# Kernel tuning notes

Hardware: AMD Instinct MI355X
Metric: run time of the kernel (lower is better)

Reference implementation:

```python
import jax, jax.numpy as jnp
import numpy as np

DIM = 128
KERNEL = 7
NUM_HEADS = 4
HEAD_DIM = DIM // NUM_HEADS
SCALE = HEAD_DIM ** (-0.5)


def _nbhd_indices(size, k):
    # NATTEN edge-clamped neighborhood: start index so the k-window stays in bounds
    pos = jnp.arange(size)
    start = jnp.clip(pos - k // 2, 0, size - k)          # (size,)
    idx = start[:, None] + jnp.arange(k)[None, :]        # (size, k) absolute key index
    bias = idx - pos[:, None] + (k - 1)                  # (size, k) rpb index in [0, 2k-2]
    return idx, bias


def setup_inputs() -> dict:
    key = jax.random.key(0)
    ks = jax.random.split(key, 6)
    B, H, W = 4, 64, 64
    x = jax.random.normal(ks[0], (B, H, W, DIM), dtype=jnp.float32)
    w_qkv = jax.random.normal(ks[1], (DIM, 3 * DIM), dtype=jnp.float32) * (DIM ** -0.5)
    b_qkv = jax.random.normal(ks[2], (3 * DIM,), dtype=jnp.float32) * 0.02
    rpb = jax.random.normal(ks[3], (NUM_HEADS, 2 * KERNEL - 1, 2 * KERNEL - 1), dtype=jnp.float32) * 0.02
    w_proj = jax.random.normal(ks[4], (DIM, DIM), dtype=jnp.float32) * (DIM ** -0.5)
    b_proj = jax.random.normal(ks[5], (DIM,), dtype=jnp.float32) * 0.02
    return {"x": x, "w_qkv": w_qkv, "b_qkv": b_qkv, "rpb": rpb,
            "w_proj": w_proj, "b_proj": b_proj}


def reference(x, w_qkv, b_qkv, rpb, w_proj, b_proj):
    B, H, W, C = x.shape
    k = KERNEL
    # qkv projection; split order (3, heads, head_dim) matches torch reshape
    qkv = (x @ w_qkv + b_qkv).reshape(B, H, W, 3, NUM_HEADS, HEAD_DIM)
    q = jnp.transpose(qkv[..., 0, :, :], (0, 3, 1, 2, 4)) * SCALE  # (B,nh,H,W,hd)
    kk = jnp.transpose(qkv[..., 1, :, :], (0, 3, 1, 2, 4))
    v = jnp.transpose(qkv[..., 2, :, :], (0, 3, 1, 2, 4))

    idx_i, bias_i = _nbhd_indices(H, k)  # (H,k)
    idx_j, bias_j = _nbhd_indices(W, k)  # (W,k)

    # gather local k x k neighborhoods of keys/values: (B,nh,H,W,k,k,hd)
    II = idx_i[:, None, :, None]
    JJ = idx_j[None, :, None, :]
    k_nb = kk[:, :, II, JJ, :]
    v_nb = v[:, :, II, JJ, :]

    # QK + relative position bias gathered per offset
    attn = jnp.einsum('bnhwd,bnhwpqd->bnhwpq', q, k_nb)
    attn = attn + rpb[:, bias_i[:, None, :, None], bias_j[None, :, None, :]][None]

    # softmax over the k*k neighborhood
    attn = jax.nn.softmax(attn.reshape(B, NUM_HEADS, H, W, k * k), axis=-1)
    attn = attn.reshape(B, NUM_HEADS, H, W, k, k)

    out = jnp.einsum('bnhwpq,bnhwpqd->bnhwd', attn, v_nb)
    out = jnp.transpose(out, (0, 2, 3, 1, 4)).reshape(B, H, W, C)
    return out @ w_proj + b_proj
```

## Files before the change

### kernel.cpp

```cpp
#include <hip/hip_runtime.h>
#include <hip/hip_bf16.h>

typedef float f4 __attribute__((ext_vector_type(4)));
typedef float f32x4 __attribute__((ext_vector_type(4)));
typedef unsigned short u16x8 __attribute__((ext_vector_type(8)));
typedef short short8 __attribute__((ext_vector_type(8)));

#define QSCALE 0.17677669529663689f

__device__ inline float b2f(unsigned short u){
  union{unsigned int i; float f;} z; z.i = ((unsigned int)u)<<16; return z.f;
}
__device__ inline unsigned short f2b(float f){
  union{float f; unsigned int i;} z; z.f=f;
  unsigned int i = z.i;
  return (unsigned short)((i + 0x7FFFu + ((i>>16)&1u)) >> 16);
}

__global__ __launch_bounds__(256) void k_prep(const float* __restrict__ wq,
    const float* __restrict__ wp, unsigned short* __restrict__ wT,
    unsigned short* __restrict__ wpT)
{
  __shared__ float T[32][129];
  const int b = blockIdx.x, t = threadIdx.x;
  const float* src; unsigned short* dst; int N, n0;
  if (b < 12){ src = wq; dst = wT;  N = 384; n0 = b*32; }
  else       { src = wp; dst = wpT; N = 128; n0 = (b-12)*32; }
  for (int i = t; i < 4096; i += 256){
    int k = i >> 5, c = i & 31;
    T[c][k] = src[k*N + n0 + c];
  }
  __syncthreads();
  const int n = t >> 3, k0 = (t & 7) << 4;
#pragma unroll
  for (int e = 0; e < 2; ++e){
    u16x8 o;
#pragma unroll
    for (int j = 0; j < 8; ++j) o[j] = f2b(T[n][k0 + e*8 + j]);
    *(u16x8*)&dst[(n0+n)*128 + k0 + e*8] = o;
  }
}

__global__ __launch_bounds__(256) void k_qkv_mfma(const float* __restrict__ x,
    const unsigned short* __restrict__ wT, const float* __restrict__ bias,
    unsigned short* __restrict__ qo, unsigned short* __restrict__ ko,
    unsigned short* __restrict__ vo)
{
  __shared__ short lds[64*128 + 128*128];
  short* As = lds;
  short* Bs = lds + 64*128;
  const int t = threadIdx.x;
  const int m0 = blockIdx.x * 64;
  const int ny = blockIdx.y;
  const int n0 = ny * 128;

  for (int c = t; c < 1024; c += 256){
    int row = c >> 4, k0 = (c & 15) << 3;
    const float* p = &x[(m0+row)*128 + k0];
    f4 lo = *(const f4*)p, hi = *(const f4*)(p+4);
    u16x8 v;
    v[0]=f2b(lo[0]); v[1]=f2b(lo[1]); v[2]=f2b(lo[2]); v[3]=f2b(lo[3]);
    v[4]=f2b(hi[0]); v[5]=f2b(hi[1]); v[6]=f2b(hi[2]); v[7]=f2b(hi[3]);
    int byte = (row<<8) + (k0<<1);
    *(u16x8*)((char*)As + (byte ^ ((row&7)<<4))) = v;
  }
  for (int c = t; c < 2048; c += 256){
    int n = c >> 4, k0 = (c & 15) << 3;
    u16x8 v = *(const u16x8*)&wT[(n0+n)*128 + k0];
    int byte = (n<<8) + (k0<<1);
    *(u16x8*)((char*)Bs + (byte ^ ((n&7)<<4))) = v;
  }
  __syncthreads();

  const int w = t >> 6, l = t & 63;
  const int wm = (w >> 1) * 32, wn = (w & 1) * 64;
  const int lr = l & 15, lk = (l >> 4) << 3;
  f32x4 acc[2][4] = {};
#pragma unroll
  for (int k0 = 0; k0 < 128; k0 += 32){
    const int koff = k0 + lk;
    short8 a[2], bf[4];
#pragma unroll
    for (int fm = 0; fm < 2; ++fm){
      int row = wm + fm*16 + lr;
      int byte = (row<<8) + (koff<<1);
      a[fm] = *(short8*)((char*)As + (byte ^ ((row&7)<<4)));
    }
#pragma unroll
    for (int fn = 0; fn < 4; ++fn){
      int rn = wn + fn*16 + lr;
      int byte = (rn<<8) + (koff<<1);
      bf[fn] = *(short8*)((char*)Bs + (byte ^ ((rn&7)<<4)));
    }
#pragma unroll
    for (int fm = 0; fm < 2; ++fm)
#pragma unroll
      for (int fn = 0; fn < 4; ++fn)
        acc[fm][fn] = __builtin_amdgcn_mfma_f32_16x16x32_bf16(a[fm], bf[fn], acc[fm][fn], 0, 0, 0);
  }
  __syncthreads();

  unsigned short* C = (unsigned short*)lds;
  const float scale = (ny == 0) ? QSCALE : 1.0f;
#pragma unroll
  for (int fm = 0; fm < 2; ++fm)
#pragma unroll
    for (int fn = 0; fn < 4; ++fn){
      int col = wn + fn*16 + lr;
      float bv = bias[n0 + col];
#pragma unroll
      for (int r = 0; r < 4; ++r){
        int row = wm + fm*16 + ((l>>4)<<2) + r;
        C[row*136 + col] = f2b((acc[fm][fn][r] + bv) * scale);
      }
    }
  __syncthreads();
  unsigned short* dst = ny==0 ? qo : (ny==1 ? ko : vo);
  for (int c = t; c < 1024; c += 256){
    int row = c >> 4, k0 = (c & 15) << 3;
    *(u16x8*)&dst[(m0+row)*128 + k0] = *(u16x8*)&C[row*136 + k0];
  }
}

__global__ __launch_bounds__(256) void k_attn(
    const unsigned short* __restrict__ qg,
    const unsigned short* __restrict__ kg,
    const unsigned short* __restrict__ vg,
    const float* __restrict__ rpb,
    unsigned short* __restrict__ ao)
{
  __shared__ unsigned short ks[196*136];
  __shared__ unsigned short vs[196*136];
  __shared__ float rs[676];
  const int t = threadIdx.x;
  const int b = blockIdx.z;
  const int th0 = blockIdx.y * 8, tw0 = blockIdx.x * 8;
  const int bi0 = min(max(th0-3,0),50);
  const int bj0 = min(max(tw0-3,0),50);
  for (int c = t; c < 3136; c += 256){
    int tok = c >> 4, part = c & 15;
    int trow = tok/14;
    int gi = bi0 + trow;
    int gj = bj0 + (tok - trow*14);
    int go = ((b*64+gi)*64+gj)*128 + part*8;
    int lo = tok*136 + part*8;
    *(u16x8*)&ks[lo] = *(const u16x8*)&kg[go];
    *(u16x8*)&vs[lo] = *(const u16x8*)&vg[go];
  }
  for (int c = t; c < 676; c += 256) rs[c] = rpb[c];
  __syncthreads();

  const int lt = t >> 2, h = t & 3;
  const int ti = th0 + (lt >> 3), tj = tw0 + (lt & 7);
  const int si = min(max(ti-3,0),57), sj = min(max(tj-3,0),57);
  const int li = si - bi0, lj = sj - bj0;
  const int ri = si - ti + 6, rj = sj - tj + 6;

  float q[32];
  {
    int qb = ((b*64+ti)*64+tj)*128 + h*32;
#pragma unroll
    for (int j=0;j<4;++j){
      u16x8 u = *(const u16x8*)&qg[qb + j*8];
#pragma unroll
      for (int e=0;e<8;++e) q[j*8+e] = b2f(u[e]);
    }
  }
  float m = -1e30f, l = 0.f, o[32];
#pragma unroll
  for (int d=0; d<32; ++d) o[d] = 0.f;

  for (int pi=0; pi<7; ++pi){
    const int rowoff = (li+pi)*14;
    const float* rrow = &rs[h*169 + (ri+pi)*13 + rj];
    for (int pj=0; pj<7; ++pj){
      int lo = (rowoff + lj + pj)*136 + h*32;
      float s = rrow[pj];
#pragma unroll
      for (int j=0;j<4;++j){
        u16x8 kk = *(const u16x8*)&ks[lo + j*8];
#pragma unroll
        for (int e=0;e<8;++e) s += q[j*8+e]*b2f(kk[e]);
      }
      float mn = fmaxf(m, s);
      float sc = __expf(m - mn);
      float e  = __expf(s - mn);
      l = l*sc + e;
#pragma unroll
      for (int j=0;j<4;++j){
        u16x8 vv = *(const u16x8*)&vs[lo + j*8];
#pragma unroll
        for (int e2=0;e2<8;++e2){
          int d = j*8+e2;
          o[d] = o[d]*sc + e*b2f(vv[e2]);
        }
      }
      m = mn;
    }
  }
  float inv = 1.f / l;
  int ob = ((b*64+ti)*64+tj)*128 + h*32;
#pragma unroll
  for (int j=0;j<16;++j){
    *(unsigned int*)&ao[ob + 2*j] =
      (unsigned int)f2b(o[2*j]*inv) | ((unsigned int)f2b(o[2*j+1]*inv)<<16);
  }
}

__global__ __launch_bounds__(256) void k_proj_mfma(
    const unsigned short* __restrict__ a,
    const unsigned short* __restrict__ wpT, const float* __restrict__ bias,
    float* __restrict__ out)
{
  __shared__ short lds[64*128 + 128*128];
  short* As = lds;
  short* Bs = lds + 64*128;
  const int t = threadIdx.x;
  const int m0 = blockIdx.x * 64;

  for (int c = t; c < 1024; c += 256){
    int row = c >> 4, k0 = (c & 15) << 3;
    u16x8 v = *(const u16x8*)&a[(m0+row)*128 + k0];
    int byte = (row<<8) + (k0<<1);
    *(u16x8*)((char*)As + (byte ^ ((row&7)<<4))) = v;
  }
  for (int c = t; c < 2048; c += 256){
    int n = c >> 4, k0 = (c & 15) << 3;
    u16x8 v = *(const u16x8*)&wpT[n*128 + k0];
    int byte = (n<<8) + (k0<<1);
    *(u16x8*)((char*)Bs + (byte ^ ((n&7)<<4))) = v;
  }
  __syncthreads();

  const int w = t >> 6, l = t & 63;
  const int wm = (w >> 1) * 32, wn = (w & 1) * 64;
  const int lr = l & 15, lk = (l >> 4) << 3;
  f32x4 acc[2][4] = {};
#pragma unroll
  for (int k0 = 0; k0 < 128; k0 += 32){
    const int koff = k0 + lk;
    short8 afr[2], bf[4];
#pragma unroll
    for (int fm = 0; fm < 2; ++fm){
      int row = wm + fm*16 + lr;
      int byte = (row<<8) + (koff<<1);
      afr[fm] = *(short8*)((char*)As + (byte ^ ((row&7)<<4)));
    }
#pragma unroll
    for (int fn = 0; fn < 4; ++fn){
      int rn = wn + fn*16 + lr;
      int byte = (rn<<8) + (koff<<1);
      bf[fn] = *(short8*)((char*)Bs + (byte ^ ((rn&7)<<4)));
    }
#pragma unroll
    for (int fm = 0; fm < 2; ++fm)
#pragma unroll
      for (int fn = 0; fn < 4; ++fn)
        acc[fm][fn] = __builtin_amdgcn_mfma_f32_16x16x32_bf16(afr[fm], bf[fn], acc[fm][fn], 0, 0, 0);
  }
  __syncthreads();

  float* C = (float*)lds;
#pragma unroll
  for (int fm = 0; fm < 2; ++fm)
#pragma unroll
    for (int fn = 0; fn < 4; ++fn){
      int col = wn + fn*16 + lr;
      float bv = bias[col];
#pragma unroll
      for (int r = 0; r < 4; ++r){
        int row = wm + fm*16 + ((l>>4)<<2) + r;
        C[row*132 + col] = acc[fm][fn][r] + bv;
      }
    }
  __syncthreads();
  for (int c = t; c < 2048; c += 256){
    int row = c >> 5, k0 = (c & 31) << 2;
    *(f4*)&out[(m0+row)*128 + k0] = *(const f4*)&C[row*132 + k0];
  }
}

extern "C" void kernel_launch(void* const* d_in, const int* in_sizes, int n_in,
                              void* d_out, int out_size, void* d_ws, size_t ws_size,
                              hipStream_t stream) {
  const float* x      = (const float*)d_in[0];
  const float* w_qkv  = (const float*)d_in[1];
  const float* b_qkv  = (const float*)d_in[2];
  const float* rpb    = (const float*)d_in[3];
  const float* w_proj = (const float*)d_in[4];
  const float* b_proj = (const float*)d_in[5];
  float* out = (float*)d_out;

  unsigned short* qo  = (unsigned short*)d_ws;
  unsigned short* ko  = qo + 16384*128;
  unsigned short* vo  = ko + 16384*128;
  unsigned short* ao  = vo + 16384*128;
  unsigned short* wT  = ao + 16384*128;
  unsigned short* wpT = wT + 384*128;

  k_prep<<<16, 256, 0, stream>>>(w_qkv, w_proj, wT, wpT);
  k_qkv_mfma<<<dim3(256, 3), 256, 0, stream>>>(x, wT, b_qkv, qo, ko, vo);
  k_attn<<<dim3(8, 8, 4), 256, 0, stream>>>(qo, ko, vo, rpb, ao);
  k_proj_mfma<<<256, 256, 0, stream>>>(ao, wpT, b_proj, out);
}
```

Before: 53.16 us.

## Split attention blocks per head with head-major QKV layout and neighbor-parallel softmax

QKV outputs are written in head-major layout, so each attention block handles a single head and loads only that head's 14x14 K/V tile into a smaller LDS buffer. The grid grows from 256 to 1024 blocks, and each token's 49 neighbors are split across 4 lanes. Each lane computes a two-pass softmax (max first, then exp-sum) instead of an online rescale, and the partial results are reduced with shuffles. This raises occupancy and parallelism and removes the serial per-neighbor rescaling, at the cost of more shuffle traffic and redundant K/V halo loads across the per-head blocks.

```diff
diff --git a/kernel.cpp b/kernel.cpp
--- a/kernel.cpp
+++ b/kernel.cpp
@@ -118,7 +118,8 @@
   unsigned short* dst = ny==0 ? qo : (ny==1 ? ko : vo);
   for (int c = t; c < 1024; c += 256){
     int row = c >> 4, k0 = (c & 15) << 3;
-    *(u16x8*)&dst[(m0+row)*128 + k0] = *(u16x8*)&C[row*136 + k0];
+    int head = k0 >> 5, d0 = k0 & 31;
+    *(u16x8*)&dst[(head*16384 + m0 + row)*32 + d0] = *(u16x8*)&C[row*136 + k0];
   }
 }
 
@@ -129,28 +130,29 @@
     const float* __restrict__ rpb,
     unsigned short* __restrict__ ao)
 {
-  __shared__ unsigned short ks[196*136];
-  __shared__ unsigned short vs[196*136];
-  __shared__ float rs[676];
+  __shared__ unsigned short ks[196*40];
+  __shared__ unsigned short vs[196*40];
+  __shared__ float rs[169];
   const int t = threadIdx.x;
-  const int b = blockIdx.z;
+  const int b = blockIdx.z >> 2, h = blockIdx.z & 3;
   const int th0 = blockIdx.y * 8, tw0 = blockIdx.x * 8;
   const int bi0 = min(max(th0-3,0),50);
   const int bj0 = min(max(tw0-3,0),50);
-  for (int c = t; c < 3136; c += 256){
-    int tok = c >> 4, part = c & 15;
-    int trow = tok/14;
-    int gi = bi0 + trow;
-    int gj = bj0 + (tok - trow*14);
-    int go = ((b*64+gi)*64+gj)*128 + part*8;
-    int lo = tok*136 + part*8;
-    *(u16x8*)&ks[lo] = *(const u16x8*)&kg[go];
-    *(u16x8*)&vs[lo] = *(const u16x8*)&vg[go];
-  }
-  for (int c = t; c < 676; c += 256) rs[c] = rpb[c];
-  __syncthreads();
-
-  const int lt = t >> 2, h = t & 3;
+  const unsigned short* kb = kg + (h*16384 + b*4096)*32;
+  const unsigned short* vb = vg + (h*16384 + b*4096)*32;
+
+  for (int c = t; c < 784; c += 256){
+    int tok = c >> 2, ch = c & 3;
+    int trow = tok/14, tcol = tok - trow*14;
+    int g = ((bi0+trow)*64 + (bj0+tcol))*32 + ch*8;
+    int lo = tok*40 + ch*8;
+    *(u16x8*)&ks[lo] = *(const u16x8*)&kb[g];
+    *(u16x8*)&vs[lo] = *(const u16x8*)&vb[g];
+  }
+  for (int c = t; c < 169; c += 256) rs[c] = rpb[h*169 + c];
+  __syncthreads();
+
+  const int lt = t >> 2, p = t & 3;
   const int ti = th0 + (lt >> 3), tj = tw0 + (lt & 7);
   const int si = min(max(ti-3,0),57), sj = min(max(tj-3,0),57);
   const int li = si - bi0, lj = sj - bj0;
@@ -158,7 +160,7 @@
 
   float q[32];
   {
-    int qb = ((b*64+ti)*64+tj)*128 + h*32;
+    int qb = (h*16384 + b*4096 + ti*64 + tj)*32;
 #pragma unroll
     for (int j=0;j<4;++j){
       u16x8 u = *(const u16x8*)&qg[qb + j*8];
@@ -166,45 +168,58 @@
       for (int e=0;e<8;++e) q[j*8+e] = b2f(u[e]);
     }
   }
-  float m = -1e30f, l = 0.f, o[32];
+
+  float s[13]; int toks[13];
+  float mx = -1e30f;
+#pragma unroll
+  for (int it = 0; it < 13; ++it){
+    int n = p + (it << 2);
+    bool ok = (n < 49);
+    int nn = ok ? n : 48;
+    int pi = nn / 7, pj = nn - pi*7;
+    int tok = (li+pi)*14 + (lj+pj);
+    toks[it] = tok;
+    float acc = rs[(ri+pi)*13 + (rj+pj)];
+#pragma unroll
+    for (int j=0;j<4;++j){
+      u16x8 kk = *(const u16x8*)&ks[tok*40 + j*8];
+#pragma unroll
+      for (int e=0;e<8;++e) acc += q[j*8+e]*b2f(kk[e]);
+    }
+    s[it] = ok ? acc : -1e30f;
+    mx = fmaxf(mx, s[it]);
+  }
+  mx = fmaxf(mx, __shfl_xor(mx, 1));
+  mx = fmaxf(mx, __shfl_xor(mx, 2));
+
+  float l = 0.f, o[32];
 #pragma unroll
   for (int d=0; d<32; ++d) o[d] = 0.f;
-
-  for (int pi=0; pi<7; ++pi){
-    const int rowoff = (li+pi)*14;
-    const float* rrow = &rs[h*169 + (ri+pi)*13 + rj];
-    for (int pj=0; pj<7; ++pj){
-      int lo = (rowoff + lj + pj)*136 + h*32;
-      float s = rrow[pj];
-#pragma unroll
-      for (int j=0;j<4;++j){
-        u16x8 kk = *(const u16x8*)&ks[lo + j*8];
-#pragma unroll
-        for (int e=0;e<8;++e) s += q[j*8+e]*b2f(kk[e]);
-      }
-      float mn = fmaxf(m, s);
-      float sc = __expf(m - mn);
-      float e  = __expf(s - mn);
-      l = l*sc + e;
-#pragma unroll
-      for (int j=0;j<4;++j){
-        u16x8 vv = *(const u16x8*)&vs[lo + j*8];
-#pragma unroll
-        for (int e2=0;e2<8;++e2){
-          int d = j*8+e2;
-          o[d] = o[d]*sc + e*b2f(vv[e2]);
-        }
-      }
-      m = mn;
-    }
-  }
+#pragma unroll
+  for (int it = 0; it < 13; ++it){
+    float e = __expf(s[it] - mx);
+    l += e;
+    int tok = toks[it];
+#pragma unroll
+    for (int j=0;j<4;++j){
+      u16x8 vv = *(const u16x8*)&vs[tok*40 + j*8];
+#pragma unroll
+      for (int e2=0;e2<8;++e2) o[j*8+e2] += e*b2f(vv[e2]);
+    }
+  }
+  l += __shfl_xor(l, 1);
+  l += __shfl_xor(l, 2);
+#pragma unroll
+  for (int d=0; d<32; ++d) o[d] += __shfl_xor(o[d], 1);
+#pragma unroll
+  for (int d=0; d<32; ++d) o[d] += __shfl_xor(o[d], 2);
+
   float inv = 1.f / l;
-  int ob = ((b*64+ti)*64+tj)*128 + h*32;
-#pragma unroll
-  for (int j=0;j<16;++j){
-    *(unsigned int*)&ao[ob + 2*j] =
-      (unsigned int)f2b(o[2*j]*inv) | ((unsigned int)f2b(o[2*j+1]*inv)<<16);
-  }
+  int ob = (b*4096 + ti*64 + tj)*128 + h*32 + p*8;
+  u16x8 w8;
+#pragma unroll
+  for (int e=0;e<8;++e) w8[e] = f2b(o[p*8+e]*inv);
+  *(u16x8*)&ao[ob] = w8;
 }
 
 __global__ __launch_bounds__(256) void k_proj_mfma(
@@ -300,6 +315,6 @@
 
   k_prep<<<16, 256, 0, stream>>>(w_qkv, w_proj, wT, wpT);
   k_qkv_mfma<<<dim3(256, 3), 256, 0, stream>>>(x, wT, b_qkv, qo, ko, vo);
-  k_attn<<<dim3(8, 8, 4), 256, 0, stream>>>(qo, ko, vo, rpb, ao);
+  k_attn<<<dim3(8, 8, 16), 256, 0, stream>>>(qo, ko, vo, rpb, ao);
   k_proj_mfma<<<256, 256, 0, stream>>>(ao, wpT, b_proj, out);
 }
```

After: 52.22 us. No clear change (-1.8%).
